# Kernel tuning notes

Hardware: AMD Instinct MI355X
Metric: run time of the kernel (lower is better)

The kernel has to match this reference:

```python
import jax, jax.numpy as jnp
import numpy as np

B, S, H, V = 64, 512, 1024, 32000


def setup_inputs() -> dict:
    key = jax.random.key(0)
    ks = jax.random.split(key, 20)
    sd = 0.02
    inp = {
        'x': jax.random.randint(ks[0], (B, 1), 0, V),
        'h_prev': jax.random.normal(ks[1], (B, H), dtype=jnp.float32),
        'annotations': jax.random.normal(ks[2], (B, S, H), dtype=jnp.float32),
        # embedding table
        'emb': jax.random.normal(ks[3], (V, H), dtype=jnp.float32) * sd,
        # attention MLP: Linear(2H -> H), ReLU, Linear(H -> 1)
        'attn_W1': jax.random.normal(ks[4], (H, 2 * H), dtype=jnp.float32) * sd,
        'attn_b1': jnp.zeros((H,), jnp.float32),
        'attn_W2': jax.random.normal(ks[5], (1, H), dtype=jnp.float32) * sd,
        'attn_b2': jnp.zeros((1,), jnp.float32),
        # GRU cell linears (input_size = 2H). NOTE: original code has a bug where
        # weights_hr is never used (r uses weights_hz); we replicate that, so no Whr.
        'W_ir': jax.random.normal(ks[6], (H, 2 * H), dtype=jnp.float32) * sd,
        'b_ir': jnp.zeros((H,), jnp.float32),
        'W_iz': jax.random.normal(ks[7], (H, 2 * H), dtype=jnp.float32) * sd,
        'b_iz': jnp.zeros((H,), jnp.float32),
        'W_in': jax.random.normal(ks[8], (H, 2 * H), dtype=jnp.float32) * sd,
        'b_in': jnp.zeros((H,), jnp.float32),
        'W_hz': jax.random.normal(ks[9], (H, H), dtype=jnp.float32) * sd,
        'b_hz': jnp.zeros((H,), jnp.float32),
        'W_hn': jax.random.normal(ks[10], (H, H), dtype=jnp.float32) * sd,
        'b_hn': jnp.zeros((H,), jnp.float32),
        # output projection H -> V
        'W_out': jax.random.normal(ks[11], (V, H), dtype=jnp.float32) * sd,
        'b_out': jnp.zeros((V,), jnp.float32),
    }
    return inp


def _lin(x, W, b):
    # torch nn.Linear: y = x @ W.T + b, W has shape (out, in)
    return x @ W.T + b


def reference(x, h_prev, annotations, emb, attn_W1, attn_b1, attn_W2, attn_b2,
              W_ir, b_ir, W_iz, b_iz, W_in, b_in, W_hz, b_hz, W_hn, b_hn,
              W_out, b_out):
    # embedding lookup, squeeze time dim: (B, H)
    embed = emb[x[:, 0]]

    # additive attention: concat(annotations, expanded hidden) -> MLP -> softmax
    # split W1 over the concat axis to avoid materializing the [B,S,2H] concat:
    # concat @ W1.T == annotations @ W1[:, :H].T + hidden @ W1[:, H:].T
    hA = jnp.einsum('bsh,kh->bsk', annotations, attn_W1[:, :H])  # (B,S,H)
    hB = h_prev @ attn_W1[:, H:].T                               # (B,H)
    hidden_act = jax.nn.relu(hA + hB[:, None, :] + attn_b1)
    scores = jnp.einsum('bsk,k->bs', hidden_act, attn_W2[0]) + attn_b2[0]
    attention_weights = jax.nn.softmax(scores, axis=1)[:, :, None]  # (B,S,1)

    # context vector
    context = jnp.sum(attention_weights * annotations, axis=1)  # (B,H)
    xc = jnp.concatenate([context, embed], axis=1)              # (B,2H)

    # GRU cell (faithful to the original, including the weights_hz reuse in r)
    hz = _lin(h_prev, W_hz, b_hz)
    z = jax.nn.sigmoid(_lin(xc, W_iz, b_iz) + hz)
    r = jax.nn.sigmoid(_lin(xc, W_ir, b_ir) + hz)  # bug replicated: uses W_hz
    g = jnp.tanh(_lin(xc, W_in, b_in) + r * _lin(h_prev, W_hn, b_hn))
    h_new = (1.0 - z) * g + z * h_prev

    output = _lin(h_new, W_out, b_out)  # (B,V)
    return output, h_new, attention_weights
```

## Files before the change

### kernel.cpp

```cpp
#include <hip/hip_runtime.h>


typedef __bf16 bf16;
typedef __attribute__((ext_vector_type(4))) float  f32x4;
typedef __attribute__((ext_vector_type(4))) float  fx4;
typedef __attribute__((ext_vector_type(8))) bf16   bf16x8;
typedef __attribute__((ext_vector_type(4))) bf16   bf16x4;
typedef __attribute__((ext_vector_type(4))) unsigned int u32x4;
typedef __attribute__((ext_vector_type(2))) unsigned int u32x2;

#define MFMA16x16x32(a, b, c) __builtin_amdgcn_mfma_f32_16x16x32_bf16(a, b, c, 0, 0, 0)

#define Bb   64
#define Ss   512
#define Hh   1024
#define Vv   32000
#define Mtot (Bb * Ss)

#define WS_HNEW_B    131072
#define WS_XC_B      262144
#define WS_W1A_B     524288
#define WS_P_HB      2621440
#define WS_P_HZ      3670016
#define WS_P_HN      4718592
#define WS_P_IZ      5767168
#define WS_P_IR      6815744
#define WS_P_IN      7864320
#define WS_SCORES    8912896
#define WS_CTX       11010048
#define WS_ANNB      13107200

#define OUT_LOGITS   0
#define OUT_HNEW     2048000
#define OUT_AW       2113536

__device__ __forceinline__ float bf2f(unsigned short u) {
    unsigned int x = ((unsigned int)u) << 16;
    float f;
    __builtin_memcpy(&f, &x, 4);
    return f;
}

__device__ __forceinline__ void gload_lds16(const bf16* g, bf16* l)
{
    __builtin_amdgcn_global_load_lds(
        (const __attribute__((address_space(1))) unsigned int*)g,
        (__attribute__((address_space(3))) unsigned int*)l,
        16, 0, 0);
}

__global__ __launch_bounds__(256, 2) void k_pre(
    const int* __restrict__ x, const float* __restrict__ h_prev,
    const float* __restrict__ emb, const float* __restrict__ attn_W1,
    const float* __restrict__ W_hz, const float* __restrict__ W_hn,
    const float* __restrict__ ann,
    bf16* __restrict__ xc_b, bf16* __restrict__ W1a_b, bf16* __restrict__ annb,
    float* __restrict__ p_hB, float* __restrict__ p_hz, float* __restrict__ p_hn)
{
    __shared__ __align__(16) bf16 lA[2][64][72];
    __shared__ __align__(16) bf16 lB[2][64][72];

    int bid = blockIdx.x, t = threadIdx.x;

    if (bid >= 1280) {
        size_t i = ((size_t)(bid - 1280) * 256 + t) * 8;
        size_t stride = (size_t)2048 * 256 * 8;
        size_t n = (size_t)Mtot * Hh;
        for (; i < n; i += stride) {
            fx4 v0 = *(const fx4*)(ann + i);
            fx4 v1 = *(const fx4*)(ann + i + 4);
            bf16x8 o;
#pragma unroll
            for (int q = 0; q < 4; q++) { o[q] = (bf16)v0[q]; o[q + 4] = (bf16)v1[q]; }
            *(bf16x8*)(annb + i) = o;
        }
        return;
    }
    if (bid >= 192) {
        int sub = bid - 192;
        if (sub < 64) {
            int b = sub, row = x[b];
            for (int i = t; i < Hh; i += 256)
                xc_b[b * 2048 + Hh + i] = (bf16)emb[(size_t)row * Hh + i];
        } else {
            int row = sub - 64;
            int k4 = t * 4;
            fx4 v = *(const fx4*)(attn_W1 + (size_t)row * 2048 + k4);
            bf16x4 o;
#pragma unroll
            for (int q = 0; q < 4; q++) o[q] = (bf16)v[q];
            *(bf16x4*)(W1a_b + (size_t)row * Hh + k4) = o;
        }
        return;
    }

    int nb = bid & 15, sk = (bid >> 4) & 3, mat = bid >> 6;
    const float* Bp = (mat == 0) ? (attn_W1 + 1024) : (mat == 1 ? W_hz : W_hn);
    int ldb         = (mat == 0) ? 2048 : 1024;
    float* op       = (mat == 0) ? p_hB : (mat == 1 ? p_hz : p_hn);

    int n0 = nb * 64, k0 = sk * 256;
    int lane = t & 63, wid = t >> 6;
    int srow = t >> 2, schunk = t & 3;

    const float* agp = h_prev + (size_t)srow * 1024 + k0 + schunk * 16;
    const float* bgp = Bp + (size_t)(n0 + srow) * ldb + k0 + schunk * 16;

    f32x4 acc[4];
#pragma unroll
    for (int i = 0; i < 4; i++) acc[i] = (f32x4)0.0f;

    fx4 aRf[4], bRf[4];
#pragma unroll
    for (int q = 0; q < 4; q++) { aRf[q] = *(const fx4*)(agp + q * 4);
                                  bRf[q] = *(const fx4*)(bgp + q * 4); }
    {
        bf16x8 a0, a1, p0, p1;
#pragma unroll
        for (int q = 0; q < 4; q++) {
            a0[q] = (bf16)aRf[0][q]; a0[q + 4] = (bf16)aRf[1][q];
            a1[q] = (bf16)aRf[2][q]; a1[q + 4] = (bf16)aRf[3][q];
            p0[q] = (bf16)bRf[0][q]; p0[q + 4] = (bf16)bRf[1][q];
            p1[q] = (bf16)bRf[2][q]; p1[q + 4] = (bf16)bRf[3][q];
        }
        *(bf16x8*)&lA[0][srow][schunk * 16]     = a0;
        *(bf16x8*)&lA[0][srow][schunk * 16 + 8] = a1;
        *(bf16x8*)&lB[0][srow][schunk * 16]     = p0;
        *(bf16x8*)&lB[0][srow][schunk * 16 + 8] = p1;
    }
    __syncthreads();

    int cur = 0;
    for (int ks = 0; ks < 4; ks++) {
        if (ks + 1 < 4) {
#pragma unroll
            for (int q = 0; q < 4; q++) {
                aRf[q] = *(const fx4*)(agp + (ks + 1) * 64 + q * 4);
                bRf[q] = *(const fx4*)(bgp + (ks + 1) * 64 + q * 4);
            }
        }
        int rA = lane & 15;
        int kc = (lane >> 4) * 8;
#pragma unroll
        for (int kk = 0; kk < 2; kk++) {
            bf16x8 bfr = *(bf16x8*)&lB[cur][wid * 16 + rA][kk * 32 + kc];
#pragma unroll
            for (int i = 0; i < 4; i++) {
                bf16x8 af = *(bf16x8*)&lA[cur][i * 16 + rA][kk * 32 + kc];
                acc[i] = MFMA16x16x32(af, bfr, acc[i]);
            }
        }
        if (ks + 1 < 4) {
            int nxt = cur ^ 1;
            bf16x8 a0, a1, p0, p1;
#pragma unroll
            for (int q = 0; q < 4; q++) {
                a0[q] = (bf16)aRf[0][q]; a0[q + 4] = (bf16)aRf[1][q];
                a1[q] = (bf16)aRf[2][q]; a1[q + 4] = (bf16)aRf[3][q];
                p0[q] = (bf16)bRf[0][q]; p0[q + 4] = (bf16)bRf[1][q];
                p1[q] = (bf16)bRf[2][q]; p1[q + 4] = (bf16)bRf[3][q];
            }
            *(bf16x8*)&lA[nxt][srow][schunk * 16]     = a0;
            *(bf16x8*)&lA[nxt][srow][schunk * 16 + 8] = a1;
            *(bf16x8*)&lB[nxt][srow][schunk * 16]     = p0;
            *(bf16x8*)&lB[nxt][srow][schunk * 16 + 8] = p1;
        }
        __syncthreads();
        cur ^= 1;
    }

    int n = n0 + wid * 16 + (lane & 15);
#pragma unroll
    for (int i = 0; i < 4; i++)
#pragma unroll
        for (int r = 0; r < 4; r++) {
            int m = i * 16 + (lane >> 4) * 4 + r;
            op[(size_t)(sk * 64 + m) * 1024 + n] = acc[i][r];
        }
}

__global__ __launch_bounds__(256, 2) void k_sgemm(
    const bf16* __restrict__ A, int lda, int kchunk,
    const float* __restrict__ B0, const float* __restrict__ B1, const float* __restrict__ B2,
    int ldb0, int ldb1, int ldb2,
    float* __restrict__ o0, float* __restrict__ o1, float* __restrict__ o2,
    const float* __restrict__ bias, int N, int finalOut)
{
    __shared__ __align__(16) bf16 lA[2][64][72];
    __shared__ __align__(16) bf16 lB[2][64][72];

    int nb = blockIdx.x, sk = blockIdx.y, mat = blockIdx.z;
    const float* Bp = (mat == 0) ? B0 : (mat == 1 ? B1 : B2);
    int ldb         = (mat == 0) ? ldb0 : (mat == 1 ? ldb1 : ldb2);
    float* op       = (mat == 0) ? o0 : (mat == 1 ? o1 : o2);

    int n0 = nb * 64, k0 = sk * kchunk;
    int t = threadIdx.x, lane = t & 63, wid = t >> 6;
    int srow = t >> 2, schunk = t & 3;

    const bf16*  agp = A  + (size_t)srow * lda + k0 + schunk * 16;
    const float* bgp = Bp + (size_t)(n0 + srow) * ldb + k0 + schunk * 16;

    f32x4 acc[4];
#pragma unroll
    for (int i = 0; i < 4; i++) acc[i] = (f32x4)0.0f;

    u32x4 aR0, aR1; fx4 bRf[4];
    int nk = kchunk >> 6;

    aR0 = *(const u32x4*)(agp);
    aR1 = *(const u32x4*)(agp + 8);
#pragma unroll
    for (int q = 0; q < 4; q++) bRf[q] = *(const fx4*)(bgp + q * 4);
    {
        *(u32x4*)&lA[0][srow][schunk * 16]     = aR0;
        *(u32x4*)&lA[0][srow][schunk * 16 + 8] = aR1;
        bf16x8 p0, p1;
#pragma unroll
        for (int q = 0; q < 4; q++) {
            p0[q] = (bf16)bRf[0][q]; p0[q + 4] = (bf16)bRf[1][q];
            p1[q] = (bf16)bRf[2][q]; p1[q + 4] = (bf16)bRf[3][q];
        }
        *(bf16x8*)&lB[0][srow][schunk * 16]     = p0;
        *(bf16x8*)&lB[0][srow][schunk * 16 + 8] = p1;
    }
    __syncthreads();

    int cur = 0;
    for (int ks = 0; ks < nk; ks++) {
        if (ks + 1 < nk) {
            aR0 = *(const u32x4*)(agp + (ks + 1) * 64);
            aR1 = *(const u32x4*)(agp + (ks + 1) * 64 + 8);
#pragma unroll
            for (int q = 0; q < 4; q++) bRf[q] = *(const fx4*)(bgp + (ks + 1) * 64 + q * 4);
        }
        int rA = lane & 15;
        int kc = (lane >> 4) * 8;
#pragma unroll
        for (int kk = 0; kk < 2; kk++) {
            bf16x8 bfr = *(bf16x8*)&lB[cur][wid * 16 + rA][kk * 32 + kc];
#pragma unroll
            for (int i = 0; i < 4; i++) {
                bf16x8 af = *(bf16x8*)&lA[cur][i * 16 + rA][kk * 32 + kc];
                acc[i] = MFMA16x16x32(af, bfr, acc[i]);
            }
        }
        if (ks + 1 < nk) {
            int nxt = cur ^ 1;
            *(u32x4*)&lA[nxt][srow][schunk * 16]     = aR0;
            *(u32x4*)&lA[nxt][srow][schunk * 16 + 8] = aR1;
            bf16x8 p0, p1;
#pragma unroll
            for (int q = 0; q < 4; q++) {
                p0[q] = (bf16)bRf[0][q]; p0[q + 4] = (bf16)bRf[1][q];
                p1[q] = (bf16)bRf[2][q]; p1[q + 4] = (bf16)bRf[3][q];
            }
            *(bf16x8*)&lB[nxt][srow][schunk * 16]     = p0;
            *(bf16x8*)&lB[nxt][srow][schunk * 16 + 8] = p1;
        }
        __syncthreads();
        cur ^= 1;
    }

    int n = n0 + wid * 16 + (lane & 15);
#pragma unroll
    for (int i = 0; i < 4; i++) {
#pragma unroll
        for (int r = 0; r < 4; r++) {
            int m = i * 16 + (lane >> 4) * 4 + r;
            float v = acc[i][r];
            if (finalOut) op[(size_t)m * N + n] = v + bias[n];
            else          op[(size_t)(sk * 64 + m) * N + n] = v;
        }
    }
}

__global__ __launch_bounds__(512, 2) void k_attn(
    const bf16* __restrict__ annb, const bf16* __restrict__ Bw,
    const float* __restrict__ p_hB, const float* __restrict__ b1,
    const float* __restrict__ W2, float* __restrict__ scores_part)
{
    extern __shared__ char smem[];

    int bid = blockIdx.x;
    int wgid = (bid & 7) * 64 + (bid >> 3);
    int mb = wgid >> 2, nbp = wgid & 3;

    int t = threadIdx.x, lane = t & 63, wid = t >> 6;
    int wm = wid >> 2, wn = wid & 3;
    int r = lane & 15, q = lane >> 4;

    const bf16* aS = annb + (size_t)mb  * 262144
                   + (size_t)(wid * 32 + (lane >> 2)) * 1024 + (lane & 3) * 8;
    const bf16* bS = Bw   + (size_t)nbp * 262144
                   + (size_t)(wid * 32 + (lane >> 2)) * 1024 + (lane & 3) * 8;
    int sld = wid * 2048;

#define STAGE(kt) do { int bq_ = ((kt) & 3) * 32768;                         \
        const bf16* a_ = aS + (kt) * 32;                                     \
        const bf16* b_ = bS + (kt) * 32;                                     \
        gload_lds16(a_,         (bf16*)(smem + bq_ + sld));                  \
        gload_lds16(a_ + 16384, (bf16*)(smem + bq_ + sld + 1024));           \
        gload_lds16(b_,         (bf16*)(smem + bq_ + 16384 + sld));          \
        gload_lds16(b_ + 16384, (bf16*)(smem + bq_ + 16384 + sld + 1024));   \
    } while (0)

    int rAo[8], rBo[4];
#pragma unroll
    for (int i = 0; i < 8; i++)
        rAo[i] = (wm * 64 + (i & 3) * 16 + (i >> 2) * 128 + r) * 64 + q * 16;
#pragma unroll
    for (int j = 0; j < 4; j++)
        rBo[j] = 16384 + (wn * 32 + (j & 1) * 16 + (j >> 1) * 128 + r) * 64 + q * 16;

    f32x4 acc[8][4];
#pragma unroll
    for (int i = 0; i < 8; i++)
#pragma unroll
        for (int j = 0; j < 4; j++) acc[i][j] = (f32x4)0.0f;

    STAGE(0); STAGE(1); STAGE(2);
    asm volatile("s_waitcnt vmcnt(8)" ::: "memory");
    __builtin_amdgcn_s_barrier();

#pragma unroll 1
    for (int kt = 0; kt < 32; kt++) {
        const char* base = smem + (kt & 3) * 32768;
        bf16x8 aq[8], bq[4];
#pragma unroll
        for (int i = 0; i < 8; i++) aq[i] = *(const bf16x8*)(base + rAo[i]);
#pragma unroll
        for (int j = 0; j < 4; j++) bq[j] = *(const bf16x8*)(base + rBo[j]);
        if (kt < 29) STAGE(kt + 3);

        __builtin_amdgcn_s_setprio(1);
#pragma unroll
        for (int i = 0; i < 8; i++)
#pragma unroll
            for (int j = 0; j < 4; j++)
                acc[i][j] = MFMA16x16x32(aq[i], bq[j], acc[i][j]);
        __builtin_amdgcn_s_setprio(0);

        if (kt < 29)       { asm volatile("s_waitcnt vmcnt(8)" ::: "memory"); }
        else if (kt == 29) { asm volatile("s_waitcnt vmcnt(4)" ::: "memory"); }
        else if (kt == 30) { asm volatile("s_waitcnt vmcnt(0)" ::: "memory"); }
        if (kt < 31) __builtin_amdgcn_s_barrier();
    }
#undef STAGE

    int m0 = mb * 256, n0g = nbp * 256;
    int b = m0 >> 9;
    float hb[4], w2v[4];
#pragma unroll
    for (int j = 0; j < 4; j++) {
        int n = n0g + (j >> 1) * 128 + wn * 32 + (j & 1) * 16 + r;
        float h = p_hB[b * Hh + n] + p_hB[65536 + b * Hh + n]
                + p_hB[131072 + b * Hh + n] + p_hB[196608 + b * Hh + n];
        hb[j]  = h + b1[n];
        w2v[j] = W2[n];
    }
    float red[32];
#pragma unroll
    for (int i = 0; i < 8; i++)
#pragma unroll
        for (int rr = 0; rr < 4; rr++) {
            float s = 0.f;
#pragma unroll
            for (int j = 0; j < 4; j++) {
                float v = acc[i][j][rr] + hb[j];
                v = fmaxf(v, 0.f);
                s += v * w2v[j];
            }
            red[i * 4 + rr] = s;
        }
#pragma unroll
    for (int mask = 1; mask <= 8; mask <<= 1)
#pragma unroll
        for (int p = 0; p < 32; p++)
            red[p] += __shfl_xor(red[p], mask, 64);

    if (r == 0) {
        float* sp = scores_part + (size_t)(nbp * 4 + wn) * Mtot;
#pragma unroll
        for (int i = 0; i < 8; i++) {
            int m = m0 + wm * 64 + (i & 3) * 16 + (i >> 2) * 128 + q * 4;
#pragma unroll
            for (int rr = 0; rr < 4; rr++)
                sp[m + rr] = red[i * 4 + rr];
        }
    }
}

__global__ void k_context(const bf16* __restrict__ annb,
                          const float* __restrict__ scores_part,
                          float* __restrict__ aw_out, float* __restrict__ ctx_part)
{
    __shared__ float law[512];
    __shared__ float red[8];
    int bid = blockIdx.x;
    int b = bid >> 3, sc = bid & 7;
    int t = threadIdx.x;
    int lane = t & 63, wid = t >> 6;

    float v0 = 0.f, v1 = 0.f;
#pragma unroll
    for (int p = 0; p < 16; p++) {
        v0 += scores_part[(size_t)p * Mtot + b * Ss + t];
        v1 += scores_part[(size_t)p * Mtot + b * Ss + t + 256];
    }
    float m = fmaxf(v0, v1);
#pragma unroll
    for (int mask = 32; mask; mask >>= 1) m = fmaxf(m, __shfl_xor(m, mask, 64));
    if (lane == 0) red[wid] = m;
    __syncthreads();
    float bm = fmaxf(fmaxf(red[0], red[1]), fmaxf(red[2], red[3]));
    float e0 = expf(v0 - bm), e1 = expf(v1 - bm);
    float ss = e0 + e1;
#pragma unroll
    for (int mask = 32; mask; mask >>= 1) ss += __shfl_xor(ss, mask, 64);
    if (lane == 0) red[4 + wid] = ss;
    __syncthreads();
    float tot = (red[4] + red[5]) + (red[6] + red[7]);
    float w0 = e0 / tot, w1 = e1 / tot;
    law[t] = w0; law[t + 256] = w1;
    if (sc == 0) {
        aw_out[b * Ss + t]       = w0;
        aw_out[b * Ss + t + 256] = w1;
    }
    __syncthreads();

    int h0 = t * 4;
    const bf16* ap = annb + (size_t)(b * Ss + sc * 64) * Hh + h0;
    float a0 = 0, a1 = 0, a2 = 0, a3 = 0;
#pragma unroll 4
    for (int s2 = 0; s2 < 64; s2++) {
        float w = law[sc * 64 + s2];
        u32x2 v = *(const u32x2*)(ap + (size_t)s2 * Hh);
        a0 += w * bf2f((unsigned short)(v[0] & 0xffff));
        a1 += w * bf2f((unsigned short)(v[0] >> 16));
        a2 += w * bf2f((unsigned short)(v[1] & 0xffff));
        a3 += w * bf2f((unsigned short)(v[1] >> 16));
    }
    fx4 o; o[0] = a0; o[1] = a1; o[2] = a2; o[3] = a3;
    *(fx4*)(ctx_part + sc * 65536 + b * Hh + h0) = o;
}

__global__ void k_xc(const float* __restrict__ ctx_part, bf16* __restrict__ xc_b)
{
    int idx = blockIdx.x * 256 + threadIdx.x;
    float c = 0.f;
#pragma unroll
    for (int p = 0; p < 8; p++) c += ctx_part[p * 65536 + idx];
    int b = idx >> 10, h = idx & 1023;
    xc_b[b * 2048 + h] = (bf16)c;
}

__global__ void k_gru(const float* __restrict__ p_iz, const float* __restrict__ p_ir,
                      const float* __restrict__ p_in, const float* __restrict__ p_hz,
                      const float* __restrict__ p_hn,
                      const float* __restrict__ b_iz, const float* __restrict__ b_ir,
                      const float* __restrict__ b_in, const float* __restrict__ b_hz,
                      const float* __restrict__ b_hn,
                      const float* __restrict__ h_prev,
                      float* __restrict__ out_h, bf16* __restrict__ h_new_b)
{
    int idx = blockIdx.x * 256 + threadIdx.x;
    int o = idx & 1023;
    float iz = p_iz[idx] + p_iz[65536 + idx] + p_iz[131072 + idx] + p_iz[196608 + idx];
    float ir = p_ir[idx] + p_ir[65536 + idx] + p_ir[131072 + idx] + p_ir[196608 + idx];
    float in_ = p_in[idx] + p_in[65536 + idx] + p_in[131072 + idx] + p_in[196608 + idx];
    float hz = p_hz[idx] + p_hz[65536 + idx] + p_hz[131072 + idx] + p_hz[196608 + idx];
    float hn = p_hn[idx] + p_hn[65536 + idx] + p_hn[131072 + idx] + p_hn[196608 + idx];
    hz += b_hz[o];
    hn += b_hn[o];
    float z = 1.f / (1.f + expf(-(iz + b_iz[o] + hz)));
    float r = 1.f / (1.f + expf(-(ir + b_ir[o] + hz)));
    float g = tanhf(in_ + b_in[o] + r * hn);
    float hp = h_prev[idx];
    float hnew = (1.f - z) * g + z * hp;
    out_h[idx] = hnew;
    h_new_b[idx] = (bf16)hnew;
}

extern "C" void kernel_launch(void* const* d_in, const int* in_sizes, int n_in,
                              void* d_out, int out_size, void* d_ws, size_t ws_size,
                              hipStream_t stream)
{
    const int*   x        = (const int*)d_in[0];
    const float* h_prev   = (const float*)d_in[1];
    const float* ann      = (const float*)d_in[2];
    const float* emb      = (const float*)d_in[3];
    const float* attn_W1  = (const float*)d_in[4];
    const float* attn_b1  = (const float*)d_in[5];
    const float* attn_W2  = (const float*)d_in[6];
    const float* W_ir     = (const float*)d_in[8];
    const float* b_ir     = (const float*)d_in[9];
    const float* W_iz     = (const float*)d_in[10];
    const float* b_iz     = (const float*)d_in[11];
    const float* W_in     = (const float*)d_in[12];
    const float* b_in     = (const float*)d_in[13];
    const float* W_hz     = (const float*)d_in[14];
    const float* b_hz     = (const float*)d_in[15];
    const float* W_hn     = (const float*)d_in[16];
    const float* b_hn     = (const float*)d_in[17];
    const float* W_out    = (const float*)d_in[18];
    const float* b_out    = (const float*)d_in[19];

    float* out = (float*)d_out;
    char*  ws  = (char*)d_ws;

    bf16*  h_new_b  = (bf16*)(ws + WS_HNEW_B);
    bf16*  xc_b     = (bf16*)(ws + WS_XC_B);
    bf16*  W1a_b    = (bf16*)(ws + WS_W1A_B);
    float* p_hB     = (float*)(ws + WS_P_HB);
    float* p_hz     = (float*)(ws + WS_P_HZ);
    float* p_hn     = (float*)(ws + WS_P_HN);
    float* p_iz     = (float*)(ws + WS_P_IZ);
    float* p_ir     = (float*)(ws + WS_P_IR);
    float* p_in     = (float*)(ws + WS_P_IN);
    float* scores_p = (float*)(ws + WS_SCORES);
    float* ctx_part = (float*)(ws + WS_CTX);
    bf16*  annb     = (bf16*)(ws + WS_ANNB);

    (void)hipFuncSetAttribute(reinterpret_cast<const void*>(k_attn),
                              hipFuncAttributeMaxDynamicSharedMemorySize, 131072);

    k_pre<<<3328, 256, 0, stream>>>(x, h_prev, emb, attn_W1, W_hz, W_hn, ann,
                                    xc_b, W1a_b, annb, p_hB, p_hz, p_hn);

    k_attn<<<512, 512, 131072, stream>>>(annb, W1a_b, p_hB, attn_b1, attn_W2,
                                         scores_p);

    k_context<<<512, 256, 0, stream>>>(annb, scores_p, out + OUT_AW, ctx_part);

    k_xc<<<256, 256, 0, stream>>>(ctx_part, xc_b);

    {
        dim3 g(16, 4, 3);
        k_sgemm<<<g, 256, 0, stream>>>(xc_b, 2048, 512,
                                       W_iz, W_ir, W_in, 2048, 2048, 2048,
                                       p_iz, p_ir, p_in, nullptr, 1024, 0);
    }

    k_gru<<<256, 256, 0, stream>>>(p_iz, p_ir, p_in, p_hz, p_hn,
                                   b_iz, b_ir, b_in, b_hz, b_hn,
                                   h_prev, out + OUT_HNEW, h_new_b);

    {
        dim3 g(500, 1, 1);
        k_sgemm<<<g, 256, 0, stream>>>(h_new_b, 1024, 1024,
                                       W_out, W_out, W_out, 1024, 1024, 1024,
                                       out + OUT_LOGITS, nullptr, nullptr,
                                       b_out, 32000, 1);
    }
}
```

Measured before the change: 166.6 us.

## Overlap W_out bf16 conversion with attention GEMM using extra warps

```diff
diff --git a/kernel.cpp b/kernel.cpp
--- a/kernel.cpp
+++ b/kernel.cpp
@@ -29,6 +29,7 @@
 #define WS_SCORES    8912896
 #define WS_CTX       11010048
 #define WS_ANNB      13107200
+#define WS_WOUTB     80216064
 
 #define OUT_LOGITS   0
 #define OUT_HNEW     2048000
@@ -275,18 +276,109 @@
     }
 }
 
-__global__ __launch_bounds__(512, 2) void k_attn(
+__global__ __launch_bounds__(256, 2) void k_sgemm_bb(
+    const bf16* __restrict__ A, const bf16* __restrict__ Bmat,
+    const float* __restrict__ bias, float* __restrict__ outp)
+{
+    __shared__ __align__(16) bf16 lA[2][64][72];
+    __shared__ __align__(16) bf16 lB[2][64][72];
+
+    int nb = blockIdx.x;
+    int n0 = nb * 64;
+    int t = threadIdx.x, lane = t & 63, wid = t >> 6;
+    int srow = t >> 2, schunk = t & 3;
+
+    const bf16* agp = A    + (size_t)srow * 1024 + schunk * 16;
+    const bf16* bgp = Bmat + (size_t)(n0 + srow) * 1024 + schunk * 16;
+
+    f32x4 acc[4];
+#pragma unroll
+    for (int i = 0; i < 4; i++) acc[i] = (f32x4)0.0f;
+
+    u32x4 aR0, aR1, bR0, bR1;
+    aR0 = *(const u32x4*)(agp);     aR1 = *(const u32x4*)(agp + 8);
+    bR0 = *(const u32x4*)(bgp);     bR1 = *(const u32x4*)(bgp + 8);
+    *(u32x4*)&lA[0][srow][schunk * 16]     = aR0;
+    *(u32x4*)&lA[0][srow][schunk * 16 + 8] = aR1;
+    *(u32x4*)&lB[0][srow][schunk * 16]     = bR0;
+    *(u32x4*)&lB[0][srow][schunk * 16 + 8] = bR1;
+    __syncthreads();
+
+    int cur = 0;
+    for (int ks = 0; ks < 16; ks++) {
+        if (ks + 1 < 16) {
+            aR0 = *(const u32x4*)(agp + (ks + 1) * 64);
+            aR1 = *(const u32x4*)(agp + (ks + 1) * 64 + 8);
+            bR0 = *(const u32x4*)(bgp + (ks + 1) * 64);
+            bR1 = *(const u32x4*)(bgp + (ks + 1) * 64 + 8);
+        }
+        int rA = lane & 15;
+        int kc = (lane >> 4) * 8;
+#pragma unroll
+        for (int kk = 0; kk < 2; kk++) {
+            bf16x8 bfr = *(bf16x8*)&lB[cur][wid * 16 + rA][kk * 32 + kc];
+#pragma unroll
+            for (int i = 0; i < 4; i++) {
+                bf16x8 af = *(bf16x8*)&lA[cur][i * 16 + rA][kk * 32 + kc];
+                acc[i] = MFMA16x16x32(af, bfr, acc[i]);
+            }
+        }
+        if (ks + 1 < 16) {
+            int nxt = cur ^ 1;
+            *(u32x4*)&lA[nxt][srow][schunk * 16]     = aR0;
+            *(u32x4*)&lA[nxt][srow][schunk * 16 + 8] = aR1;
+            *(u32x4*)&lB[nxt][srow][schunk * 16]     = bR0;
+            *(u32x4*)&lB[nxt][srow][schunk * 16 + 8] = bR1;
+        }
+        __syncthreads();
+        cur ^= 1;
+    }
+
+    int n = n0 + wid * 16 + (lane & 15);
+#pragma unroll
+    for (int i = 0; i < 4; i++) {
+#pragma unroll
+        for (int r = 0; r < 4; r++) {
+            int m = i * 16 + (lane >> 4) * 4 + r;
+            outp[(size_t)m * Vv + n] = acc[i][r] + bias[n];
+        }
+    }
+}
+
+__global__ __launch_bounds__(768, 3) void k_attn(
     const bf16* __restrict__ annb, const bf16* __restrict__ Bw,
     const float* __restrict__ p_hB, const float* __restrict__ b1,
-    const float* __restrict__ W2, float* __restrict__ scores_part)
+    const float* __restrict__ W2, float* __restrict__ scores_part,
+    const float* __restrict__ W_out, bf16* __restrict__ woutb)
 {
     extern __shared__ char smem[];
 
     int bid = blockIdx.x;
+    int t = threadIdx.x;
+
+    if (t >= 512) {
+        int rt = t - 512;
+        size_t base = ((size_t)bid * 256 + rt) * 8;
+#pragma unroll 1
+        for (int it = 0; it < 32; it++) {
+            size_t off = (size_t)it * 1048576 + base;
+            if (off < (size_t)Vv * Hh) {
+                fx4 v0 = *(const fx4*)(W_out + off);
+                fx4 v1 = *(const fx4*)(W_out + off + 4);
+                bf16x8 o;
+#pragma unroll
+                for (int q = 0; q < 4; q++) { o[q] = (bf16)v0[q]; o[q + 4] = (bf16)v1[q]; }
+                *(bf16x8*)(woutb + off) = o;
+            }
+            __builtin_amdgcn_s_barrier();
+        }
+        return;
+    }
+
     int wgid = (bid & 7) * 64 + (bid >> 3);
     int mb = wgid >> 2, nbp = wgid & 3;
 
-    int t = threadIdx.x, lane = t & 63, wid = t >> 6;
+    int lane = t & 63, wid = t >> 6;
     int wm = wid >> 2, wn = wid & 3;
     int r = lane & 15, q = lane >> 4;
 
@@ -521,6 +613,7 @@
     float* scores_p = (float*)(ws + WS_SCORES);
     float* ctx_part = (float*)(ws + WS_CTX);
     bf16*  annb     = (bf16*)(ws + WS_ANNB);
+    bf16*  woutb    = (bf16*)(ws + WS_WOUTB);
 
     (void)hipFuncSetAttribute(reinterpret_cast<const void*>(k_attn),
                               hipFuncAttributeMaxDynamicSharedMemorySize, 131072);
@@ -528,8 +621,8 @@
     k_pre<<<3328, 256, 0, stream>>>(x, h_prev, emb, attn_W1, W_hz, W_hn, ann,
                                     xc_b, W1a_b, annb, p_hB, p_hz, p_hn);
 
-    k_attn<<<512, 512, 131072, stream>>>(annb, W1a_b, p_hB, attn_b1, attn_W2,
-                                         scores_p);
+    k_attn<<<512, 768, 131072, stream>>>(annb, W1a_b, p_hB, attn_b1, attn_W2,
+                                         scores_p, W_out, woutb);
 
     k_context<<<512, 256, 0, stream>>>(annb, scores_p, out + OUT_AW, ctx_part);
 
@@ -546,11 +639,5 @@
                                    b_iz, b_ir, b_in, b_hz, b_hn,
                                    h_prev, out + OUT_HNEW, h_new_b);
 
-    {
-        dim3 g(500, 1, 1);
-        k_sgemm<<<g, 256, 0, stream>>>(h_new_b, 1024, 1024,
-                                       W_out, W_out, W_out, 1024, 1024, 1024,
-                                       out + OUT_LOGITS, nullptr, nullptr,
-                                       b_out, 32000, 1);
-    }
-}
+    k_sgemm_bb<<<500, 256, 0, stream>>>(h_new_b, woutb, b_out, out + OUT_LOGITS);
+}
```

New measurement: 406.3 us. 2.44x slower.
